# Kernel tuning notes

Hardware: AMD Instinct MI355X
Metric: run time of the kernel (lower is better)

The kernel has to match this reference:

```python
import jax, jax.numpy as jnp
import numpy as np

B, NAG = 8192, 16          # scenes, agents per scene
CIN, CH = 64, 128          # gnn_in_channels, gnn_out_channels
R2 = 8.0 * 8.0             # comm_range squared
BOX = 20.0                 # positions sampled uniformly in [0, BOX]^2


def _lin(k, fi, fo):
    k1, k2 = jax.random.split(k)
    s = 1.0 / np.sqrt(fi)
    W = jax.random.uniform(k1, (fi, fo), jnp.float32, -s, s)
    b = jax.random.uniform(k2, (fo,), jnp.float32, -s, s)
    return W, b


def setup_inputs() -> dict:
    key = jax.random.key(0)
    ks = jax.random.split(key, 10)
    x = jax.random.normal(ks[0], (B * NAG, CIN), jnp.float32)          # VAE mu per agent
    pos = jax.random.uniform(ks[1], (B, NAG, 2), jnp.float32) * BOX    # sensor xy positions
    W_rel1, b_rel1 = _lin(ks[2], CIN, CH)
    W_root1, _ = _lin(ks[3], CIN, CH)
    W_rel2, b_rel2 = _lin(ks[4], CH, CH)
    W_root2, _ = _lin(ks[5], CH, CH)
    Wh1, bh1 = _lin(ks[6], 2 * CH, 64)
    Wh2, bh2 = _lin(ks[7], 64, 32)
    Wh3, bh3 = _lin(ks[8], 32, 16)
    return dict(x=x, pos=pos, W_rel1=W_rel1, b_rel1=b_rel1, W_root1=W_root1,
                W_rel2=W_rel2, b_rel2=b_rel2, W_root2=W_root2,
                Wh1=Wh1, bh1=bh1, Wh2=Wh2, bh2=bh2, Wh3=Wh3, bh3=bh3)


def _graph_conv(h, adj, W_rel, b_rel, W_root):
    # PyG GraphConv (aggr='add'): out_i = W_rel @ sum_{j in N(i)} h_j + b_rel + W_root @ h_i
    nb = adj.shape[0]
    hb = h.reshape(nb, NAG, h.shape[-1])                 # [B, n, C]
    agg = jnp.einsum('bij,bjc->bic', adj, hb)            # neighbor sum within each scene
    return agg.reshape(h.shape[0], -1) @ W_rel + b_rel + h @ W_root


def reference(x, pos, W_rel1, b_rel1, W_root1, W_rel2, b_rel2, W_root2,
              Wh1, bh1, Wh2, bh2, Wh3, bh3):
    # radius_graph (batch-isolated, loop=False) as a per-scene dense mask
    diff = pos[:, :, None, :] - pos[:, None, :, :]       # [B, n, n, 2]
    d2 = jnp.sum(diff * diff, axis=-1)                   # [B, n, n]
    eye = jnp.eye(NAG, dtype=bool)
    adj = ((d2 <= R2) & ~eye).astype(x.dtype)            # [B, n, n]
    # Dropout(p=0.2) omitted (eval / deterministic reference).
    x1 = jax.nn.relu(_graph_conv(x, adj, W_rel1, b_rel1, W_root1))   # named 'x1' (inplace ReLU)
    x2 = jax.nn.relu(_graph_conv(x1, adj, W_rel2, b_rel2, W_root2))  # named 'x2' (inplace ReLU)
    h = jnp.concatenate([x1, x2], axis=-1)               # JumpingKnowledge('cat')
    h = jax.nn.relu(h @ Wh1 + bh1)
    h = jax.nn.relu(h @ Wh2 + bh2)
    out = h @ Wh3 + bh3                                  # [N, 16]
    return out.reshape(B, NAG, 16)
```

## Files before the change

kernel.cpp:

```cpp
#include <hip/hip_runtime.h>

#define NSCENE 8192
#define NAG 16
#define R2f 64.0f

typedef unsigned short u16;
typedef __attribute__((ext_vector_type(8))) short short8;
typedef __attribute__((ext_vector_type(4))) float f32x4;

#define OFF_B1 0
#define OFF_B2 16384
#define OFF_H1 49152
#define OFF_H2 65536
#define OFF_H3 67584
#define SWZ_UNITS 8512

__device__ __forceinline__ u16 f2b(float f) {
    unsigned u = __float_as_uint(f);
    unsigned r = u + 0x7FFFu + ((u >> 16) & 1u);
    return (u16)(r >> 16);
}

__global__ __launch_bounds__(256) void swizzle_w(
    const float* __restrict__ Wrel1, const float* __restrict__ Wroot1,
    const float* __restrict__ Wrel2, const float* __restrict__ Wroot2,
    const float* __restrict__ Wh1,  const float* __restrict__ Wh2,
    const float* __restrict__ Wh3,  u16* __restrict__ ws)
{
    const int u = blockIdx.x * 256 + threadIdx.x;
    if (u >= SWZ_UNITS) return;

    int v, T, N, ksplit;
    const float *W, *W2;
    u16* dst;
    if (u < 2048)      { v = u;        T = 8; N = 128; ksplit = 64;  W = Wroot1; W2 = Wrel1; dst = ws + OFF_B1 + v * 8; }
    else if (u < 6144) { v = u - 2048; T = 8; N = 128; ksplit = 128; W = Wroot2; W2 = Wrel2; dst = ws + OFF_B2 + v * 8; }
    else if (u < 8192) { v = u - 6144; T = 4; N = 64;  ksplit = 1 << 30; W = Wh1; W2 = Wh1; dst = ws + OFF_H1 + v * 8; }
    else if (u < 8448) { v = u - 8192; T = 2; N = 32;  ksplit = 1 << 30; W = Wh2; W2 = Wh2; dst = ws + OFF_H2 + v * 8; }
    else               { v = u - 8448; T = 1; N = 16;  ksplit = 1 << 30; W = Wh3; W2 = Wh3; dst = ws + OFF_H3 + v * 8; }

    const int lane = v & 63;
    const int t = (v >> 6) % T;
    const int s = (v >> 6) / T;
    const int n = t * 16 + (lane & 15);
    const int k0 = s * 32 + (lane >> 4) * 8;
    #pragma unroll
    for (int j = 0; j < 8; ++j) {
        const int k = k0 + j;
        const float val = (k < ksplit) ? W[k * N + n] : W2[(k - ksplit) * N + n];
        dst[j] = f2b(val);
    }
}

__device__ __forceinline__ void unpack2(unsigned w, float& a, float& b) {
    a = __uint_as_float(w << 16);
    b = __uint_as_float(w & 0xFFFF0000u);
}

__global__ __launch_bounds__(256) void gnn_mfma(
    const float* __restrict__ x, const float* __restrict__ pos,
    const float* __restrict__ brel1, const float* __restrict__ brel2,
    const float* __restrict__ bh1,  const float* __restrict__ bh2,
    const float* __restrict__ bh3,
    const u16* __restrict__ ws, float* __restrict__ out)
{
    __shared__ __align__(16) u16 XA[16 * 136];
    __shared__ __align__(16) u16 X12[16 * 272];
    __shared__ __align__(16) u16 X2s[16 * 136];
    __shared__ __align__(16) u16 H1s[16 * 72];
    __shared__ __align__(16) u16 H2s[16 * 48];
    __shared__ unsigned mask[NAG];

    const int t = threadIdx.x;
    const int scene = blockIdx.x;
    const int wv = t >> 6;
    const int lane = t & 63;
    const int mrow = lane & 15;
    const int q = lane >> 4;

    {
        const int i0 = t * 4;
        const float4 v = *(const float4*)(x + scene * (NAG * 64) + i0);
        u16* d = &XA[(i0 >> 6) * 136 + (i0 & 63)];
        d[0] = f2b(v.x); d[1] = f2b(v.y); d[2] = f2b(v.z); d[3] = f2b(v.w);
    }
    if (t < NAG) {
        const float* pp = pos + scene * (NAG * 2);
        const float ax = pp[2 * t], ay = pp[2 * t + 1];
        unsigned m = 0;
        for (int j = 0; j < NAG; ++j) {
            const float dx = ax - pp[2 * j], dy = ay - pp[2 * j + 1];
            if (dx * dx + dy * dy <= R2f && j != t) m |= (1u << j);
        }
        mask[t] = m;
    }
    __syncthreads();

    {
        const int a = t >> 4, c0 = (t & 15) * 4;
        const unsigned m = mask[a];
        float s0 = 0.f, s1 = 0.f, s2 = 0.f, s3 = 0.f;
        for (int j = 0; j < NAG; ++j) {
            const unsigned* p = (const unsigned*)&XA[j * 136 + c0];
            float f0, f1, f2, f3;
            unpack2(p[0], f0, f1); unpack2(p[1], f2, f3);
            const bool on = (m >> j) & 1;
            s0 += on ? f0 : 0.f; s1 += on ? f1 : 0.f;
            s2 += on ? f2 : 0.f; s3 += on ? f3 : 0.f;
        }
        u16* d = &XA[a * 136 + 64 + c0];
        d[0] = f2b(s0); d[1] = f2b(s1); d[2] = f2b(s2); d[3] = f2b(s3);
    }
    __syncthreads();

    {
        const float bias0 = brel1[wv * 32 + mrow];
        const float bias1 = brel1[wv * 32 + 16 + mrow];
        f32x4 acc0 = {0.f, 0.f, 0.f, 0.f}, acc1 = acc0;
        #pragma unroll
        for (int s = 0; s < 4; ++s) {
            const short8 a = *(const short8*)&XA[mrow * 136 + s * 32 + q * 8];
            const short8 b0 = *(const short8*)&ws[OFF_B1 + ((s * 8 + 2 * wv) * 64 + lane) * 8];
            const short8 b1 = *(const short8*)&ws[OFF_B1 + ((s * 8 + 2 * wv + 1) * 64 + lane) * 8];
            acc0 = __builtin_amdgcn_mfma_f32_16x16x32_bf16(a, b0, acc0, 0, 0, 0);
            acc1 = __builtin_amdgcn_mfma_f32_16x16x32_bf16(a, b1, acc1, 0, 0, 0);
        }
        #pragma unroll
        for (int r = 0; r < 4; ++r) {
            const int row = q * 4 + r;
            float v0 = acc0[r] + bias0; v0 = v0 > 0.f ? v0 : 0.f;
            float v1 = acc1[r] + bias1; v1 = v1 > 0.f ? v1 : 0.f;
            X12[row * 272 + wv * 32 + mrow] = f2b(v0);
            X12[row * 272 + wv * 32 + 16 + mrow] = f2b(v1);
        }
    }
    __syncthreads();

    {
        const int a = t >> 4, c0 = (t & 15) * 8;
        const unsigned m = mask[a];
        float s0=0.f,s1=0.f,s2=0.f,s3=0.f,s4=0.f,s5=0.f,s6=0.f,s7=0.f;
        for (int j = 0; j < NAG; ++j) {
            const unsigned* p = (const unsigned*)&X12[j * 272 + c0];
            float f0,f1,f2,f3,f4,f5,f6,f7;
            unpack2(p[0], f0, f1); unpack2(p[1], f2, f3);
            unpack2(p[2], f4, f5); unpack2(p[3], f6, f7);
            const bool on = (m >> j) & 1;
            s0 += on ? f0 : 0.f; s1 += on ? f1 : 0.f; s2 += on ? f2 : 0.f; s3 += on ? f3 : 0.f;
            s4 += on ? f4 : 0.f; s5 += on ? f5 : 0.f; s6 += on ? f6 : 0.f; s7 += on ? f7 : 0.f;
        }
        u16* d = &X12[a * 272 + 128 + c0];
        d[0]=f2b(s0); d[1]=f2b(s1); d[2]=f2b(s2); d[3]=f2b(s3);
        d[4]=f2b(s4); d[5]=f2b(s5); d[6]=f2b(s6); d[7]=f2b(s7);
    }
    __syncthreads();

    {
        const float bias0 = brel2[wv * 32 + mrow];
        const float bias1 = brel2[wv * 32 + 16 + mrow];
        f32x4 acc0 = {0.f, 0.f, 0.f, 0.f}, acc1 = acc0;
        #pragma unroll
        for (int s = 0; s < 8; ++s) {
            const short8 a = *(const short8*)&X12[mrow * 272 + s * 32 + q * 8];
            const short8 b0 = *(const short8*)&ws[OFF_B2 + ((s * 8 + 2 * wv) * 64 + lane) * 8];
            const short8 b1 = *(const short8*)&ws[OFF_B2 + ((s * 8 + 2 * wv + 1) * 64 + lane) * 8];
            acc0 = __builtin_amdgcn_mfma_f32_16x16x32_bf16(a, b0, acc0, 0, 0, 0);
            acc1 = __builtin_amdgcn_mfma_f32_16x16x32_bf16(a, b1, acc1, 0, 0, 0);
        }
        #pragma unroll
        for (int r = 0; r < 4; ++r) {
            const int row = q * 4 + r;
            float v0 = acc0[r] + bias0; v0 = v0 > 0.f ? v0 : 0.f;
            float v1 = acc1[r] + bias1; v1 = v1 > 0.f ? v1 : 0.f;
            X2s[row * 136 + wv * 32 + mrow] = f2b(v0);
            X2s[row * 136 + wv * 32 + 16 + mrow] = f2b(v1);
        }
    }
    __syncthreads();

    {
        const float bias = bh1[wv * 16 + mrow];
        f32x4 acc = {0.f, 0.f, 0.f, 0.f};
        #pragma unroll
        for (int s = 0; s < 8; ++s) {
            const short8 a = (s < 4)
                ? *(const short8*)&X12[mrow * 272 + s * 32 + q * 8]
                : *(const short8*)&X2s[mrow * 136 + (s - 4) * 32 + q * 8];
            const short8 b = *(const short8*)&ws[OFF_H1 + ((s * 4 + wv) * 64 + lane) * 8];
            acc = __builtin_amdgcn_mfma_f32_16x16x32_bf16(a, b, acc, 0, 0, 0);
        }
        #pragma unroll
        for (int r = 0; r < 4; ++r) {
            float v = acc[r] + bias; v = v > 0.f ? v : 0.f;
            H1s[(q * 4 + r) * 72 + wv * 16 + mrow] = f2b(v);
        }
    }
    __syncthreads();

    if (wv < 2) {
        const float bias = bh2[wv * 16 + mrow];
        f32x4 acc = {0.f, 0.f, 0.f, 0.f};
        #pragma unroll
        for (int s = 0; s < 2; ++s) {
            const short8 a = *(const short8*)&H1s[mrow * 72 + s * 32 + q * 8];
            const short8 b = *(const short8*)&ws[OFF_H2 + ((s * 2 + wv) * 64 + lane) * 8];
            acc = __builtin_amdgcn_mfma_f32_16x16x32_bf16(a, b, acc, 0, 0, 0);
        }
        #pragma unroll
        for (int r = 0; r < 4; ++r) {
            float v = acc[r] + bias; v = v > 0.f ? v : 0.f;
            H2s[(q * 4 + r) * 48 + wv * 16 + mrow] = f2b(v);
        }
    }
    __syncthreads();

    if (wv == 0) {
        const float bias = bh3[mrow];
        f32x4 acc = {0.f, 0.f, 0.f, 0.f};
        const short8 a = *(const short8*)&H2s[mrow * 48 + q * 8];
        const short8 b = *(const short8*)&ws[OFF_H3 + lane * 8];
        acc = __builtin_amdgcn_mfma_f32_16x16x32_bf16(a, b, acc, 0, 0, 0);
        float* o = out + scene * (NAG * 16);
        #pragma unroll
        for (int r = 0; r < 4; ++r)
            o[(q * 4 + r) * 16 + mrow] = acc[r] + bias;
    }
}

extern "C" void kernel_launch(void* const* d_in, const int* in_sizes, int n_in,
                              void* d_out, int out_size, void* d_ws, size_t ws_size,
                              hipStream_t stream) {
    const float* x      = (const float*)d_in[0];
    const float* pos    = (const float*)d_in[1];
    const float* Wrel1  = (const float*)d_in[2];
    const float* brel1  = (const float*)d_in[3];
    const float* Wroot1 = (const float*)d_in[4];
    const float* Wrel2  = (const float*)d_in[5];
    const float* brel2  = (const float*)d_in[6];
    const float* Wroot2 = (const float*)d_in[7];
    const float* Wh1    = (const float*)d_in[8];
    const float* bh1    = (const float*)d_in[9];
    const float* Wh2    = (const float*)d_in[10];
    const float* bh2    = (const float*)d_in[11];
    const float* Wh3    = (const float*)d_in[12];
    const float* bh3    = (const float*)d_in[13];
    u16* ws = (u16*)d_ws;

    swizzle_w<<<(SWZ_UNITS + 255) / 256, 256, 0, stream>>>(
        Wrel1, Wroot1, Wrel2, Wroot2, Wh1, Wh2, Wh3, ws);
    gnn_mfma<<<NSCENE, 256, 0, stream>>>(
        x, pos, brel1, brel2, bh1, bh2, bh3, ws, (float*)d_out);
}
```

Baseline: 146.1 us.

## Process four scenes per block and run neighbor aggregation on MFMA

Each block now handles four scenes (64 agents), so weight fragments loaded from global memory are reused across four M-tiles instead of one. Neighbor sums are computed with MFMA using a block-diagonal adjacency built from the bitmasks, replacing the scalar masked-add loops. Biases are folded into the accumulator initialisation. The cost is a larger shared-memory pool (about 79 KB), which limits resident blocks per CU, plus more registers for the cached fragments.

```diff
diff --git a/kernel.cpp b/kernel.cpp
--- a/kernel.cpp
+++ b/kernel.cpp
@@ -1,12 +1,15 @@
 #include <hip/hip_runtime.h>
 
-#define NSCENE 8192
 #define NAG 16
+#define SPB 4
+#define NBLK 2048
 #define R2f 64.0f
 
 typedef unsigned short u16;
 typedef __attribute__((ext_vector_type(8))) short short8;
 typedef __attribute__((ext_vector_type(4))) float f32x4;
+
+#define MFMA(a, b, c) __builtin_amdgcn_mfma_f32_16x16x32_bf16(a, b, c, 0, 0, 0)
 
 #define OFF_B1 0
 #define OFF_B2 16384
@@ -52,178 +55,261 @@
     }
 }
 
-__device__ __forceinline__ void unpack2(unsigned w, float& a, float& b) {
-    a = __uint_as_float(w << 16);
-    b = __uint_as_float(w & 0xFFFF0000u);
-}
-
-__global__ __launch_bounds__(256) void gnn_mfma(
+__device__ __forceinline__ short8 ldfrag(const u16* __restrict__ ws, int off,
+                                         int T, int s, int tile, int lane) {
+    return *(const short8*)(ws + off + (size_t)(((s * T + tile) * 64 + lane) * 8));
+}
+
+__device__ __forceinline__ short8 make_adjA(unsigned m, int q, int odd) {
+    union { short8 v; unsigned u[4]; } r;
+    const bool on = (q >> 1) == odd;
+    const int base = (q & 1) * 8;
+    #pragma unroll
+    for (int jj = 0; jj < 4; ++jj) {
+        const int k0 = base + 2 * jj;
+        const unsigned lo = (on && ((m >> k0) & 1u)) ? 0x3F80u : 0u;
+        const unsigned hi = (on && ((m >> (k0 + 1)) & 1u)) ? 0x3F80u : 0u;
+        r.u[jj] = lo | (hi << 16);
+    }
+    return r.v;
+}
+
+__device__ __forceinline__ void relu_store4(u16* d, f32x4 a) {
+    const unsigned p0 = (unsigned)f2b(fmaxf(a[0], 0.f)) | ((unsigned)f2b(fmaxf(a[1], 0.f)) << 16);
+    const unsigned p1 = (unsigned)f2b(fmaxf(a[2], 0.f)) | ((unsigned)f2b(fmaxf(a[3], 0.f)) << 16);
+    uint2 u; u.x = p0; u.y = p1;
+    *(uint2*)d = u;
+}
+
+__global__ __launch_bounds__(256) void gnn_fused4(
     const float* __restrict__ x, const float* __restrict__ pos,
     const float* __restrict__ brel1, const float* __restrict__ brel2,
     const float* __restrict__ bh1,  const float* __restrict__ bh2,
     const float* __restrict__ bh3,
     const u16* __restrict__ ws, float* __restrict__ out)
 {
-    __shared__ __align__(16) u16 XA[16 * 136];
-    __shared__ __align__(16) u16 X12[16 * 272];
-    __shared__ __align__(16) u16 X2s[16 * 136];
-    __shared__ __align__(16) u16 H1s[16 * 72];
-    __shared__ __align__(16) u16 H2s[16 * 48];
-    __shared__ unsigned mask[NAG];
+    __shared__ __align__(16) u16 pool[39424];
+    __shared__ unsigned mask[64];
+    u16* const xcat = pool;
+    u16* const xT   = pool + 8704;
+    u16* const xc2  = pool + 13312;
+    u16* const x1T  = pool + 30208;
+    u16* const x2b  = pool;
+    u16* const h1b  = pool + 8704;
+    u16* const h2b  = pool + 30208;
 
     const int t = threadIdx.x;
-    const int scene = blockIdx.x;
-    const int wv = t >> 6;
-    const int lane = t & 63;
-    const int mrow = lane & 15;
-    const int q = lane >> 4;
-
-    {
-        const int i0 = t * 4;
-        const float4 v = *(const float4*)(x + scene * (NAG * 64) + i0);
-        u16* d = &XA[(i0 >> 6) * 136 + (i0 & 63)];
-        d[0] = f2b(v.x); d[1] = f2b(v.y); d[2] = f2b(v.z); d[3] = f2b(v.w);
-    }
-    if (t < NAG) {
-        const float* pp = pos + scene * (NAG * 2);
-        const float ax = pp[2 * t], ay = pp[2 * t + 1];
+    const int wv = t >> 6, lane = t & 63, ln = lane & 15, q = lane >> 4;
+    const size_t sA = (size_t)blockIdx.x * SPB;
+
+    {
+        const int r = t >> 2;
+        const int co = (t & 3) * 16;
+        const float* src = x + (sA * 16 + r) * 64 + co;
+        const float4 v0 = *(const float4*)(src);
+        const float4 v1 = *(const float4*)(src + 4);
+        const float4 v2 = *(const float4*)(src + 8);
+        const float4 v3 = *(const float4*)(src + 12);
+        u16 h[16];
+        h[0] = f2b(v0.x); h[1] = f2b(v0.y); h[2]  = f2b(v0.z); h[3]  = f2b(v0.w);
+        h[4] = f2b(v1.x); h[5] = f2b(v1.y); h[6]  = f2b(v1.z); h[7]  = f2b(v1.w);
+        h[8] = f2b(v2.x); h[9] = f2b(v2.y); h[10] = f2b(v2.z); h[11] = f2b(v2.w);
+        h[12]= f2b(v3.x); h[13]= f2b(v3.y); h[14] = f2b(v3.z); h[15] = f2b(v3.w);
+        uint4 ua, ub;
+        ua.x = (unsigned)h[0]  | ((unsigned)h[1]  << 16);
+        ua.y = (unsigned)h[2]  | ((unsigned)h[3]  << 16);
+        ua.z = (unsigned)h[4]  | ((unsigned)h[5]  << 16);
+        ua.w = (unsigned)h[6]  | ((unsigned)h[7]  << 16);
+        ub.x = (unsigned)h[8]  | ((unsigned)h[9]  << 16);
+        ub.y = (unsigned)h[10] | ((unsigned)h[11] << 16);
+        ub.z = (unsigned)h[12] | ((unsigned)h[13] << 16);
+        ub.w = (unsigned)h[14] | ((unsigned)h[15] << 16);
+        *(uint4*)&xcat[r * 136 + co]     = ua;
+        *(uint4*)&xcat[r * 136 + co + 8] = ub;
+        #pragma unroll
+        for (int i = 0; i < 16; ++i)
+            xT[(co + i) * 72 + r] = h[i];
+    }
+    if (t < 64) {
+        const int g = t >> 4, a = t & 15;
+        const float* pp = pos + (sA + g) * (NAG * 2);
+        const float ax = pp[2 * a], ay = pp[2 * a + 1];
         unsigned m = 0;
         for (int j = 0; j < NAG; ++j) {
             const float dx = ax - pp[2 * j], dy = ay - pp[2 * j + 1];
-            if (dx * dx + dy * dy <= R2f && j != t) m |= (1u << j);
-        }
-        mask[t] = m;
-    }
-    __syncthreads();
-
-    {
-        const int a = t >> 4, c0 = (t & 15) * 4;
-        const unsigned m = mask[a];
-        float s0 = 0.f, s1 = 0.f, s2 = 0.f, s3 = 0.f;
-        for (int j = 0; j < NAG; ++j) {
-            const unsigned* p = (const unsigned*)&XA[j * 136 + c0];
-            float f0, f1, f2, f3;
-            unpack2(p[0], f0, f1); unpack2(p[1], f2, f3);
-            const bool on = (m >> j) & 1;
-            s0 += on ? f0 : 0.f; s1 += on ? f1 : 0.f;
-            s2 += on ? f2 : 0.f; s3 += on ? f3 : 0.f;
-        }
-        u16* d = &XA[a * 136 + 64 + c0];
-        d[0] = f2b(s0); d[1] = f2b(s1); d[2] = f2b(s2); d[3] = f2b(s3);
-    }
-    __syncthreads();
-
-    {
-        const float bias0 = brel1[wv * 32 + mrow];
-        const float bias1 = brel1[wv * 32 + 16 + mrow];
-        f32x4 acc0 = {0.f, 0.f, 0.f, 0.f}, acc1 = acc0;
+            if (dx * dx + dy * dy <= R2f && j != a) m |= (1u << j);
+        }
+        mask[g * 16 + a] = m;
+    }
+    __syncthreads();
+
+    {
+        const int nt = wv;
+        const short8 B0 = *(const short8*)&xT[(nt * 16 + ln) * 72 + q * 8];
+        const short8 B1 = *(const short8*)&xT[(nt * 16 + ln) * 72 + 32 + q * 8];
+        #pragma unroll
+        for (int g = 0; g < 4; ++g) {
+            const short8 A = make_adjA(mask[g * 16 + ln], q, g & 1);
+            f32x4 acc = {0.f, 0.f, 0.f, 0.f};
+            acc = MFMA(A, (g < 2) ? B0 : B1, acc);
+            #pragma unroll
+            for (int r = 0; r < 4; ++r)
+                xcat[(g * 16 + q * 4 + r) * 136 + 64 + nt * 16 + ln] = f2b(acc[r]);
+        }
+    }
+    __syncthreads();
+
+    {
+        const int n0 = 2 * wv, n1 = 2 * wv + 1;
+        short8 Bf0[4], Bf1[4];
         #pragma unroll
         for (int s = 0; s < 4; ++s) {
-            const short8 a = *(const short8*)&XA[mrow * 136 + s * 32 + q * 8];
-            const short8 b0 = *(const short8*)&ws[OFF_B1 + ((s * 8 + 2 * wv) * 64 + lane) * 8];
-            const short8 b1 = *(const short8*)&ws[OFF_B1 + ((s * 8 + 2 * wv + 1) * 64 + lane) * 8];
-            acc0 = __builtin_amdgcn_mfma_f32_16x16x32_bf16(a, b0, acc0, 0, 0, 0);
-            acc1 = __builtin_amdgcn_mfma_f32_16x16x32_bf16(a, b1, acc1, 0, 0, 0);
-        }
-        #pragma unroll
-        for (int r = 0; r < 4; ++r) {
-            const int row = q * 4 + r;
-            float v0 = acc0[r] + bias0; v0 = v0 > 0.f ? v0 : 0.f;
-            float v1 = acc1[r] + bias1; v1 = v1 > 0.f ? v1 : 0.f;
-            X12[row * 272 + wv * 32 + mrow] = f2b(v0);
-            X12[row * 272 + wv * 32 + 16 + mrow] = f2b(v1);
-        }
-    }
-    __syncthreads();
-
-    {
-        const int a = t >> 4, c0 = (t & 15) * 8;
-        const unsigned m = mask[a];
-        float s0=0.f,s1=0.f,s2=0.f,s3=0.f,s4=0.f,s5=0.f,s6=0.f,s7=0.f;
-        for (int j = 0; j < NAG; ++j) {
-            const unsigned* p = (const unsigned*)&X12[j * 272 + c0];
-            float f0,f1,f2,f3,f4,f5,f6,f7;
-            unpack2(p[0], f0, f1); unpack2(p[1], f2, f3);
-            unpack2(p[2], f4, f5); unpack2(p[3], f6, f7);
-            const bool on = (m >> j) & 1;
-            s0 += on ? f0 : 0.f; s1 += on ? f1 : 0.f; s2 += on ? f2 : 0.f; s3 += on ? f3 : 0.f;
-            s4 += on ? f4 : 0.f; s5 += on ? f5 : 0.f; s6 += on ? f6 : 0.f; s7 += on ? f7 : 0.f;
-        }
-        u16* d = &X12[a * 272 + 128 + c0];
-        d[0]=f2b(s0); d[1]=f2b(s1); d[2]=f2b(s2); d[3]=f2b(s3);
-        d[4]=f2b(s4); d[5]=f2b(s5); d[6]=f2b(s6); d[7]=f2b(s7);
-    }
-    __syncthreads();
-
-    {
-        const float bias0 = brel2[wv * 32 + mrow];
-        const float bias1 = brel2[wv * 32 + 16 + mrow];
-        f32x4 acc0 = {0.f, 0.f, 0.f, 0.f}, acc1 = acc0;
+            Bf0[s] = ldfrag(ws, OFF_B1, 8, s, n0, lane);
+            Bf1[s] = ldfrag(ws, OFF_B1, 8, s, n1, lane);
+        }
+        const float b0 = brel1[n0 * 16 + ln], b1 = brel1[n1 * 16 + ln];
+        #pragma unroll
+        for (int m = 0; m < 4; ++m) {
+            short8 Af[4];
+            #pragma unroll
+            for (int s = 0; s < 4; ++s)
+                Af[s] = *(const short8*)&xcat[(m * 16 + ln) * 136 + s * 32 + q * 8];
+            f32x4 a0 = {b0, b0, b0, b0}, a1 = {b1, b1, b1, b1};
+            #pragma unroll
+            for (int s = 0; s < 4; ++s) {
+                a0 = MFMA(Af[s], Bf0[s], a0);
+                a1 = MFMA(Af[s], Bf1[s], a1);
+            }
+            #pragma unroll
+            for (int r = 0; r < 4; ++r) {
+                const int row = m * 16 + q * 4 + r;
+                xc2[row * 264 + n0 * 16 + ln] = f2b(fmaxf(a0[r], 0.f));
+                xc2[row * 264 + n1 * 16 + ln] = f2b(fmaxf(a1[r], 0.f));
+            }
+            relu_store4(&x1T[(n0 * 16 + ln) * 72 + m * 16 + q * 4], a0);
+            relu_store4(&x1T[(n1 * 16 + ln) * 72 + m * 16 + q * 4], a1);
+        }
+    }
+    __syncthreads();
+
+    {
+        const int n0 = 2 * wv, n1 = 2 * wv + 1;
+        short8 B00 = *(const short8*)&x1T[(n0 * 16 + ln) * 72 + q * 8];
+        short8 B01 = *(const short8*)&x1T[(n0 * 16 + ln) * 72 + 32 + q * 8];
+        short8 B10 = *(const short8*)&x1T[(n1 * 16 + ln) * 72 + q * 8];
+        short8 B11 = *(const short8*)&x1T[(n1 * 16 + ln) * 72 + 32 + q * 8];
+        #pragma unroll
+        for (int g = 0; g < 4; ++g) {
+            const short8 A = make_adjA(mask[g * 16 + ln], q, g & 1);
+            f32x4 a0 = {0.f, 0.f, 0.f, 0.f}, a1 = a0;
+            a0 = MFMA(A, (g < 2) ? B00 : B01, a0);
+            a1 = MFMA(A, (g < 2) ? B10 : B11, a1);
+            #pragma unroll
+            for (int r = 0; r < 4; ++r) {
+                const int row = g * 16 + q * 4 + r;
+                xc2[row * 264 + 128 + n0 * 16 + ln] = f2b(a0[r]);
+                xc2[row * 264 + 128 + n1 * 16 + ln] = f2b(a1[r]);
+            }
+        }
+    }
+    __syncthreads();
+
+    {
+        const int n0 = 2 * wv, n1 = 2 * wv + 1;
+        short8 Bf0[8], Bf1[8];
         #pragma unroll
         for (int s = 0; s < 8; ++s) {
-            const short8 a = *(const short8*)&X12[mrow * 272 + s * 32 + q * 8];
-            const short8 b0 = *(const short8*)&ws[OFF_B2 + ((s * 8 + 2 * wv) * 64 + lane) * 8];
-            const short8 b1 = *(const short8*)&ws[OFF_B2 + ((s * 8 + 2 * wv + 1) * 64 + lane) * 8];
-            acc0 = __builtin_amdgcn_mfma_f32_16x16x32_bf16(a, b0, acc0, 0, 0, 0);
-            acc1 = __builtin_amdgcn_mfma_f32_16x16x32_bf16(a, b1, acc1, 0, 0, 0);
-        }
-        #pragma unroll
-        for (int r = 0; r < 4; ++r) {
-            const int row = q * 4 + r;
-            float v0 = acc0[r] + bias0; v0 = v0 > 0.f ? v0 : 0.f;
-            float v1 = acc1[r] + bias1; v1 = v1 > 0.f ? v1 : 0.f;
-            X2s[row * 136 + wv * 32 + mrow] = f2b(v0);
-            X2s[row * 136 + wv * 32 + 16 + mrow] = f2b(v1);
-        }
-    }
-    __syncthreads();
-
-    {
-        const float bias = bh1[wv * 16 + mrow];
-        f32x4 acc = {0.f, 0.f, 0.f, 0.f};
-        #pragma unroll
-        for (int s = 0; s < 8; ++s) {
-            const short8 a = (s < 4)
-                ? *(const short8*)&X12[mrow * 272 + s * 32 + q * 8]
-                : *(const short8*)&X2s[mrow * 136 + (s - 4) * 32 + q * 8];
-            const short8 b = *(const short8*)&ws[OFF_H1 + ((s * 4 + wv) * 64 + lane) * 8];
-            acc = __builtin_amdgcn_mfma_f32_16x16x32_bf16(a, b, acc, 0, 0, 0);
-        }
-        #pragma unroll
-        for (int r = 0; r < 4; ++r) {
-            float v = acc[r] + bias; v = v > 0.f ? v : 0.f;
-            H1s[(q * 4 + r) * 72 + wv * 16 + mrow] = f2b(v);
-        }
-    }
-    __syncthreads();
-
-    if (wv < 2) {
-        const float bias = bh2[wv * 16 + mrow];
-        f32x4 acc = {0.f, 0.f, 0.f, 0.f};
-        #pragma unroll
-        for (int s = 0; s < 2; ++s) {
-            const short8 a = *(const short8*)&H1s[mrow * 72 + s * 32 + q * 8];
-            const short8 b = *(const short8*)&ws[OFF_H2 + ((s * 2 + wv) * 64 + lane) * 8];
-            acc = __builtin_amdgcn_mfma_f32_16x16x32_bf16(a, b, acc, 0, 0, 0);
-        }
-        #pragma unroll
-        for (int r = 0; r < 4; ++r) {
-            float v = acc[r] + bias; v = v > 0.f ? v : 0.f;
-            H2s[(q * 4 + r) * 48 + wv * 16 + mrow] = f2b(v);
-        }
-    }
-    __syncthreads();
-
-    if (wv == 0) {
-        const float bias = bh3[mrow];
-        f32x4 acc = {0.f, 0.f, 0.f, 0.f};
-        const short8 a = *(const short8*)&H2s[mrow * 48 + q * 8];
-        const short8 b = *(const short8*)&ws[OFF_H3 + lane * 8];
-        acc = __builtin_amdgcn_mfma_f32_16x16x32_bf16(a, b, acc, 0, 0, 0);
-        float* o = out + scene * (NAG * 16);
+            Bf0[s] = ldfrag(ws, OFF_B2, 8, s, n0, lane);
+            Bf1[s] = ldfrag(ws, OFF_B2, 8, s, n1, lane);
+        }
+        const float b0 = brel2[n0 * 16 + ln], b1 = brel2[n1 * 16 + ln];
+        #pragma unroll
+        for (int m = 0; m < 4; ++m) {
+            short8 Af[8];
+            #pragma unroll
+            for (int s = 0; s < 8; ++s)
+                Af[s] = *(const short8*)&xc2[(m * 16 + ln) * 264 + s * 32 + q * 8];
+            f32x4 a0 = {b0, b0, b0, b0}, a1 = {b1, b1, b1, b1};
+            f32x4 c0 = {0.f, 0.f, 0.f, 0.f}, c1 = c0;
+            #pragma unroll
+            for (int s = 0; s < 4; ++s) {
+                a0 = MFMA(Af[s], Bf0[s], a0);
+                a1 = MFMA(Af[s], Bf1[s], a1);
+                c0 = MFMA(Af[s + 4], Bf0[s + 4], c0);
+                c1 = MFMA(Af[s + 4], Bf1[s + 4], c1);
+            }
+            #pragma unroll
+            for (int r = 0; r < 4; ++r) {
+                const int row = m * 16 + q * 4 + r;
+                x2b[row * 136 + n0 * 16 + ln] = f2b(fmaxf(a0[r] + c0[r], 0.f));
+                x2b[row * 136 + n1 * 16 + ln] = f2b(fmaxf(a1[r] + c1[r], 0.f));
+            }
+        }
+    }
+    __syncthreads();
+
+    {
+        const int nt = wv;
+        short8 Bf[8];
+        #pragma unroll
+        for (int s = 0; s < 8; ++s)
+            Bf[s] = ldfrag(ws, OFF_H1, 4, s, nt, lane);
+        const float b = bh1[nt * 16 + ln];
+        #pragma unroll
+        for (int m = 0; m < 4; ++m) {
+            short8 Af[8];
+            #pragma unroll
+            for (int s = 0; s < 4; ++s)
+                Af[s] = *(const short8*)&xc2[(m * 16 + ln) * 264 + s * 32 + q * 8];
+            #pragma unroll
+            for (int s = 0; s < 4; ++s)
+                Af[s + 4] = *(const short8*)&x2b[(m * 16 + ln) * 136 + s * 32 + q * 8];
+            f32x4 a = {b, b, b, b}, c = {0.f, 0.f, 0.f, 0.f};
+            #pragma unroll
+            for (int s = 0; s < 4; ++s) {
+                a = MFMA(Af[s], Bf[s], a);
+                c = MFMA(Af[s + 4], Bf[s + 4], c);
+            }
+            #pragma unroll
+            for (int r = 0; r < 4; ++r)
+                h1b[(m * 16 + q * 4 + r) * 72 + nt * 16 + ln] = f2b(fmaxf(a[r] + c[r], 0.f));
+        }
+    }
+    __syncthreads();
+
+    {
+        const int nt = wv & 1;
+        const int m0 = (wv >> 1) * 2;
+        short8 Bf[2];
+        Bf[0] = ldfrag(ws, OFF_H2, 2, 0, nt, lane);
+        Bf[1] = ldfrag(ws, OFF_H2, 2, 1, nt, lane);
+        const float b = bh2[nt * 16 + ln];
+        #pragma unroll
+        for (int mi = 0; mi < 2; ++mi) {
+            const int m = m0 + mi;
+            const short8 A0 = *(const short8*)&h1b[(m * 16 + ln) * 72 + q * 8];
+            const short8 A1 = *(const short8*)&h1b[(m * 16 + ln) * 72 + 32 + q * 8];
+            f32x4 a = {b, b, b, b};
+            a = MFMA(A0, Bf[0], a);
+            a = MFMA(A1, Bf[1], a);
+            #pragma unroll
+            for (int r = 0; r < 4; ++r)
+                h2b[(m * 16 + q * 4 + r) * 40 + nt * 16 + ln] = f2b(fmaxf(a[r], 0.f));
+        }
+    }
+    __syncthreads();
+
+    {
+        const int m = wv;
+        const short8 A = *(const short8*)&h2b[(m * 16 + ln) * 40 + q * 8];
+        const short8 B = ldfrag(ws, OFF_H3, 1, 0, 0, lane);
+        const float b = bh3[ln];
+        f32x4 a = {b, b, b, b};
+        a = MFMA(A, B, a);
+        float* o = out + (sA * 16 + m * 16) * 16;
         #pragma unroll
         for (int r = 0; r < 4; ++r)
-            o[(q * 4 + r) * 16 + mrow] = acc[r] + bias;
+            o[(q * 4 + r) * 16 + ln] = a[r];
     }
 }
 
@@ -248,6 +334,6 @@
 
     swizzle_w<<<(SWZ_UNITS + 255) / 256, 256, 0, stream>>>(
         Wrel1, Wroot1, Wrel2, Wroot2, Wh1, Wh2, Wh3, ws);
-    gnn_mfma<<<NSCENE, 256, 0, stream>>>(
+    gnn_fused4<<<NBLK, 256, 0, stream>>>(
         x, pos, brel1, brel2, bh1, bh2, bh3, ws, (float*)d_out);
 }
```

Result: faster. 135.6 us (-7.2%).
